# Kernel tuning notes

Hardware: AMD Instinct MI355X
Metric: run time of the kernel (lower is better)

The kernel has to match this reference:

```python
import jax, jax.numpy as jnp
import numpy as np
from jax import lax

B, T, D, R, V = 128, 8, 2048, 4, 512

def setup_inputs() -> dict:
    key = jax.random.key(0)
    k0, k1, k2, k3, k4 = jax.random.split(key, 5)
    # scales chosen so the TT products stay within fp32 range (see notes)
    input_embs = jax.random.normal(k0, (B, T, D), dtype=jnp.float32) * 0.1
    label_ids = jax.random.randint(k1, (B, T), 0, V)
    w_alpha = jax.random.normal(k2, (D, R), dtype=jnp.float32) * 0.04
    w_beta = jax.random.normal(k3, (D, R), dtype=jnp.float32) * 0.04
    w_vocab = jax.random.normal(k4, (D, V * R * R), dtype=jnp.float32) * 0.04
    return {"input_embs": input_embs, "label_ids": label_ids,
            "w_alpha": w_alpha, "w_beta": w_beta, "w_vocab": w_vocab}

def _tt_loss(input_embs, w_alpha, w_beta, w_vocab, label_ids):
    b, t, d = input_embs.shape
    flat = input_embs.reshape(-1, d)                    # [B*T, D]
    alpha = jnp.abs((flat @ w_alpha).reshape(b, t, R).mean(1))   # [B, R]
    beta = jnp.abs((flat @ w_beta).reshape(b, t, R).mean(1))     # [B, R]
    core = jnp.abs((flat @ w_vocab).reshape(b, t, R, V, R).mean(1))  # [B, R, V, R]

    # --- _select: gather per-position R x R cores and chain-multiply ---
    core_v = core.transpose(0, 2, 1, 3)                 # [B, V, R, R]
    sel = jnp.take_along_axis(core_v, label_ids[:, :, None, None], axis=1)  # [B, T, R, R]
    sel_t = jnp.swapaxes(sel, 0, 1)                     # [T, B, R, R]

    def chain(carry, m):
        return jnp.einsum('bik,bkj->bij', carry, m), None
    res, _ = lax.scan(chain, sel_t[0], sel_t[1:])       # [B, R, R]
    u = jnp.einsum('bi,bij,bj->b', alpha, res, beta)    # unnormalized probs [B]

    # --- normalization constant: marg^(T+1) contracted with alpha/beta ---
    marg = core.sum(2)                                  # [B, R, R]

    def pow_step(c, _):
        return jnp.einsum('bik,bkj->bij', c, marg), None
    zmat, _ = lax.scan(pow_step, marg, None, length=t)  # marg^(t+1)
    z = jnp.einsum('bi,bij,bj->b', alpha, zmat, beta)

    loss = -jnp.log(u / z)
    return loss.mean()

def reference(input_embs, label_ids, w_alpha, w_beta, w_vocab):
    return _tt_loss(input_embs, w_alpha, w_beta, w_vocab, label_ids)
```

## Files before the change

### kernel.cpp

```cpp
#include <hip/hip_runtime.h>
#include <math.h>

#define BB 128
#define TT 8
#define DD 2048
#define RR 4
#define VV 512

typedef __attribute__((ext_vector_type(8))) short short8;
typedef __attribute__((ext_vector_type(4))) float v4f;

#define BARSYNC() asm volatile("s_waitcnt lgkmcnt(0)\n\ts_barrier" ::: "memory")

__device__ __forceinline__ unsigned pack_bf16(float x, float y) {
    union { float f; unsigned u; } a, b;
    a.f = x; b.f = y;
    unsigned ua = a.u + 0x7fffu + ((a.u >> 16) & 1u);
    unsigned ub = b.u + 0x7fffu + ((b.u >> 16) & 1u);
    return (ua >> 16) | (ub & 0xffff0000u);
}

__global__ __launch_bounds__(256) void phaseA(const float* __restrict__ inp,
                                              const float* __restrict__ w_alpha,
                                              const float* __restrict__ w_beta,
                                              unsigned short* __restrict__ fmb,
                                              float* __restrict__ alphaP,
                                              float* __restrict__ betaP,
                                              float* __restrict__ marg) {
    int bid = blockIdx.x;
    int b = bid >> 1, half = bid & 1;
    int tid = threadIdx.x;

    if (bid < 8) marg[bid * 256 + tid] = 0.f;

    const float* base = inp + (size_t)b * TT * DD;
    float pa[4] = {0.f, 0.f, 0.f, 0.f};
    float pb[4] = {0.f, 0.f, 0.f, 0.f};
#pragma unroll
    for (int i = 0; i < 4; ++i) {
        int d = half * 1024 + i * 256 + tid;
        float s = 0.f;
#pragma unroll
        for (int t = 0; t < TT; ++t) s += base[t * DD + d];
        float v = s * (1.0f / TT);
        union { float f; unsigned u; } cv; cv.f = v;
        unsigned r = cv.u + 0x7fffu + ((cv.u >> 16) & 1u);
        fmb[b * DD + d] = (unsigned short)(r >> 16);
        float4 wa = *(const float4*)(w_alpha + d * 4);
        float4 wb = *(const float4*)(w_beta + d * 4);
        pa[0] += v * wa.x; pa[1] += v * wa.y; pa[2] += v * wa.z; pa[3] += v * wa.w;
        pb[0] += v * wb.x; pb[1] += v * wb.y; pb[2] += v * wb.z; pb[3] += v * wb.w;
    }
#pragma unroll
    for (int r = 0; r < 4; ++r) {
        for (int m = 1; m < 64; m <<= 1) {
            pa[r] += __shfl_xor(pa[r], m);
            pb[r] += __shfl_xor(pb[r], m);
        }
    }
    __shared__ float sA[4][4], sB[4][4];
    int wid = tid >> 6;
    if ((tid & 63) == 0) {
#pragma unroll
        for (int r = 0; r < 4; ++r) { sA[wid][r] = pa[r]; sB[wid][r] = pb[r]; }
    }
    __syncthreads();
    if (tid < 4) {
        alphaP[b * 8 + half * 4 + tid] = sA[0][tid] + sA[1][tid] + sA[2][tid] + sA[3][tid];
        betaP [b * 8 + half * 4 + tid] = sB[0][tid] + sB[1][tid] + sB[2][tid] + sB[3][tid];
    }
}

__global__ __launch_bounds__(512, 2) void phaseB(const unsigned short* __restrict__ fmb,
                                                 const float* __restrict__ wv,
                                                 const int* __restrict__ labels,
                                                 float* __restrict__ margA,
                                                 float* __restrict__ sel) {
    __shared__ unsigned short Ws[4][32][136];
    __shared__ int slab[BB * TT];

    const int tid = threadIdx.x;
    const int nb = blockIdx.x;
    const int col0 = nb * 32;

    slab[tid] = labels[tid];
    slab[tid + 512] = labels[tid + 512];

    const int nq = tid & 7;
    const int kp = tid >> 3;
    const int w = tid >> 6;
    const int lane = tid & 63;
    const int m15 = lane & 15;
    const int q = lane >> 4;

    const float* wbase = wv + (size_t)(2 * kp) * 8192 + col0 + nq * 4;
    const unsigned short* abase = fmb + (w * 16 + m15) * DD + q * 8;

    v4f acc0 = {0.f, 0.f, 0.f, 0.f};
    v4f acc1 = {0.f, 0.f, 0.f, 0.f};
    short8 afr[2][4];
    float4 sw[3][2];

#pragma unroll
    for (int c = 0; c < 3; ++c) {
        const float* p = wbase + (size_t)c * 128 * 8192;
        sw[c][0] = *(const float4*)(p);
        sw[c][1] = *(const float4*)(p + 8192);
    }
#pragma unroll
    for (int ks = 0; ks < 4; ++ks) afr[0][ks] = *(const short8*)(abase + ks * 32);
#pragma unroll
    for (int c = 0; c < 2; ++c) {
        const float* f0 = (const float*)&sw[c][0];
        const float* f1 = (const float*)&sw[c][1];
#pragma unroll
        for (int j = 0; j < 4; ++j)
            *(unsigned*)&Ws[c][nq * 4 + j][2 * kp] = pack_bf16(f0[j], f1[j]);
    }
    BARSYNC();

#pragma unroll
    for (int c = 0; c < 16; ++c) {
        if (c + 3 < 16) {
            const float* p = wbase + (size_t)(c + 3) * 128 * 8192;
            sw[c % 3][0] = *(const float4*)(p);
            sw[c % 3][1] = *(const float4*)(p + 8192);
        }
        if (c + 1 < 16) {
            const unsigned short* ap = abase + (c + 1) * 128;
#pragma unroll
            for (int ks = 0; ks < 4; ++ks) afr[(c + 1) & 1][ks] = *(const short8*)(ap + ks * 32);
        }
#pragma unroll
        for (int ks = 0; ks < 4; ++ks) {
            short8 b0 = *(const short8*)&Ws[c & 3][m15][ks * 32 + q * 8];
            short8 b1 = *(const short8*)&Ws[c & 3][16 + m15][ks * 32 + q * 8];
            acc0 = __builtin_amdgcn_mfma_f32_16x16x32_bf16(afr[c & 1][ks], b0, acc0, 0, 0, 0);
            acc1 = __builtin_amdgcn_mfma_f32_16x16x32_bf16(afr[c & 1][ks], b1, acc1, 0, 0, 0);
        }
        if (c + 2 < 16) {
            const float* f0 = (const float*)&sw[(c + 2) % 3][0];
            const float* f1 = (const float*)&sw[(c + 2) % 3][1];
#pragma unroll
            for (int j = 0; j < 4; ++j)
                *(unsigned*)&Ws[(c + 2) & 3][nq * 4 + j][2 * kp] = pack_bf16(f0[j], f1[j]);
        }
        if (c & 1) BARSYNC();
    }

    const int vbase = (nb & 63) * 8;
    const int iblk = nb >> 6;
    const int j = m15 & 3;
    const int v0 = vbase + (m15 >> 2);
    const float* a0p = (const float*)&acc0;
    const float* a1p = (const float*)&acc1;
#pragma unroll
    for (int r = 0; r < 4; ++r) {
        int m = w * 16 + q * 4 + r;
        float a0 = fabsf(a0p[r]);
        float a1 = fabsf(a1p[r]);
        float s = a0 + a1;
        s += __shfl_xor(s, 4);
        s += __shfl_xor(s, 8);
        if ((lane & 12) == 0) atomicAdd(&margA[m * 16 + iblk * 4 + j], s);
#pragma unroll
        for (int t = 0; t < TT; ++t) {
            int lv = slab[m * 8 + t];
            if (lv == v0)     sel[(m * 8 + t) * 16 + iblk * 4 + j] = a0;
            if (lv == v0 + 4) sel[(m * 8 + t) * 16 + iblk * 4 + j] = a1;
        }
    }
}

__global__ __launch_bounds__(128) void phaseD(const float* __restrict__ alphaP,
                                              const float* __restrict__ betaP,
                                              const float* __restrict__ marg,
                                              const float* __restrict__ sel,
                                              float* __restrict__ out) {
    int b = threadIdx.x;
    const float* sb = sel + b * TT * 16;
    float res[16], tmp[16], mm[16], zm[16];
#pragma unroll
    for (int e = 0; e < 16; ++e) res[e] = sb[e];
    for (int t = 1; t < TT; ++t) {
        const float* m = sb + t * 16;
#pragma unroll
        for (int i = 0; i < 4; ++i)
#pragma unroll
            for (int jj = 0; jj < 4; ++jj) {
                float s = 0.f;
#pragma unroll
                for (int k = 0; k < 4; ++k) s += res[i * 4 + k] * m[k * 4 + jj];
                tmp[i * 4 + jj] = s;
            }
#pragma unroll
        for (int e = 0; e < 16; ++e) res[e] = tmp[e];
    }
#pragma unroll
    for (int e = 0; e < 16; ++e) { mm[e] = marg[b * 16 + e]; zm[e] = mm[e]; }
    for (int st = 0; st < TT; ++st) {
#pragma unroll
        for (int i = 0; i < 4; ++i)
#pragma unroll
            for (int jj = 0; jj < 4; ++jj) {
                float s = 0.f;
#pragma unroll
                for (int k = 0; k < 4; ++k) s += zm[i * 4 + k] * mm[k * 4 + jj];
                tmp[i * 4 + jj] = s;
            }
#pragma unroll
        for (int e = 0; e < 16; ++e) zm[e] = tmp[e];
    }
    float u = 0.f, z = 0.f;
#pragma unroll
    for (int i = 0; i < 4; ++i) {
        float ai = fabsf(alphaP[b * 8 + i] + alphaP[b * 8 + 4 + i]);
#pragma unroll
        for (int jj = 0; jj < 4; ++jj) {
            float bj = fabsf(betaP[b * 8 + jj] + betaP[b * 8 + 4 + jj]);
            u += ai * res[i * 4 + jj] * bj;
            z += ai * zm[i * 4 + jj] * bj;
        }
    }
    float loss = logf(z) - logf(u);
    __shared__ float red[128];
    red[b] = loss;
    __syncthreads();
    for (int off = 64; off >= 1; off >>= 1) {
        if (b < off) red[b] += red[b + off];
        __syncthreads();
    }
    if (b == 0) out[0] = red[0] * (1.0f / BB);
}

extern "C" void kernel_launch(void* const* d_in, const int* in_sizes, int n_in,
                              void* d_out, int out_size, void* d_ws, size_t ws_size,
                              hipStream_t stream) {
    const float* inp     = (const float*)d_in[0];
    const int*   labels  = (const int*)d_in[1];
    const float* w_alpha = (const float*)d_in[2];
    const float* w_beta  = (const float*)d_in[3];
    const float* wv      = (const float*)d_in[4];
    float* out = (float*)d_out;

    float* ws     = (float*)d_ws;
    float* alphaP = ws;
    float* betaP  = ws + 1024;
    float* marg   = ws + 2048;
    float* sel    = ws + 4096;
    unsigned short* fmb = (unsigned short*)(ws + 20480);

    phaseA<<<256, 256, 0, stream>>>(inp, w_alpha, w_beta, fmb, alphaP, betaP, marg);
    phaseB<<<256, 512, 0, stream>>>(fmb, wv, labels, marg, sel);
    phaseD<<<1, 128, 0, stream>>>(alphaP, betaP, marg, sel, out);
}
```

Before: 124.4 us.

## Use inline-asm global loads with explicit vmcnt waits and double-buffered LDS

```diff
diff --git a/kernel.cpp b/kernel.cpp
--- a/kernel.cpp
+++ b/kernel.cpp
@@ -11,6 +11,13 @@
 typedef __attribute__((ext_vector_type(4))) float v4f;
 
 #define BARSYNC() asm volatile("s_waitcnt lgkmcnt(0)\n\ts_barrier" ::: "memory")
+
+__device__ __forceinline__ void gl4f(float4& d, const float* p) {
+    asm volatile("global_load_dwordx4 %0, %1, off" : "=v"(d) : "v"(p));
+}
+__device__ __forceinline__ void gl4s(short8& d, const unsigned short* p) {
+    asm volatile("global_load_dwordx4 %0, %1, off" : "=v"(d) : "v"(p));
+}
 
 __device__ __forceinline__ unsigned pack_bf16(float x, float y) {
     union { float f; unsigned u; } a, b;
@@ -76,7 +83,7 @@
                                                  const int* __restrict__ labels,
                                                  float* __restrict__ margA,
                                                  float* __restrict__ sel) {
-    __shared__ unsigned short Ws[4][32][136];
+    __shared__ unsigned short Ws[2][32][136];
     __shared__ int slab[BB * TT];
 
     const int tid = threadIdx.x;
@@ -99,53 +106,63 @@
     v4f acc0 = {0.f, 0.f, 0.f, 0.f};
     v4f acc1 = {0.f, 0.f, 0.f, 0.f};
     short8 afr[2][4];
-    float4 sw[3][2];
-
-#pragma unroll
-    for (int c = 0; c < 3; ++c) {
-        const float* p = wbase + (size_t)c * 128 * 8192;
-        sw[c][0] = *(const float4*)(p);
-        sw[c][1] = *(const float4*)(p + 8192);
-    }
-#pragma unroll
-    for (int ks = 0; ks < 4; ++ks) afr[0][ks] = *(const short8*)(abase + ks * 32);
-#pragma unroll
-    for (int c = 0; c < 2; ++c) {
-        const float* f0 = (const float*)&sw[c][0];
-        const float* f1 = (const float*)&sw[c][1];
+    float4 sw[2][2];
+
+    gl4f(sw[0][0], wbase);
+    gl4f(sw[0][1], wbase + 8192);
+    {
+        const float* p = wbase + (size_t)128 * 8192;
+        gl4f(sw[1][0], p);
+        gl4f(sw[1][1], p + 8192);
+    }
+#pragma unroll
+    for (int ks = 0; ks < 4; ++ks) gl4s(afr[0][ks], abase + ks * 32);
+
+    asm volatile("s_waitcnt vmcnt(6)" ::: "memory");
+    __builtin_amdgcn_sched_barrier(0);
+    {
+        const float* f0 = (const float*)&sw[0][0];
+        const float* f1 = (const float*)&sw[0][1];
 #pragma unroll
         for (int j = 0; j < 4; ++j)
-            *(unsigned*)&Ws[c][nq * 4 + j][2 * kp] = pack_bf16(f0[j], f1[j]);
+            *(unsigned*)&Ws[0][nq * 4 + j][2 * kp] = pack_bf16(f0[j], f1[j]);
     }
     BARSYNC();
 
 #pragma unroll
     for (int c = 0; c < 16; ++c) {
-        if (c + 3 < 16) {
-            const float* p = wbase + (size_t)(c + 3) * 128 * 8192;
-            sw[c % 3][0] = *(const float4*)(p);
-            sw[c % 3][1] = *(const float4*)(p + 8192);
+        const int P = c & 1, Q = 1 - P;
+        if (c + 2 < 16) {
+            const float* p = wbase + (size_t)(c + 2) * 128 * 8192;
+            gl4f(sw[P][0], p);
+            gl4f(sw[P][1], p + 8192);
         }
         if (c + 1 < 16) {
             const unsigned short* ap = abase + (c + 1) * 128;
-#pragma unroll
-            for (int ks = 0; ks < 4; ++ks) afr[(c + 1) & 1][ks] = *(const short8*)(ap + ks * 32);
-        }
+            gl4s(afr[Q][0], ap);
+            gl4s(afr[Q][1], ap + 32);
+            gl4s(afr[Q][2], ap + 64);
+            gl4s(afr[Q][3], ap + 96);
+        }
+        if (c <= 13)      asm volatile("s_waitcnt vmcnt(6)" ::: "memory");
+        else if (c == 14) asm volatile("s_waitcnt vmcnt(4)" ::: "memory");
+        else              asm volatile("s_waitcnt vmcnt(0)" ::: "memory");
+        __builtin_amdgcn_sched_barrier(0);
 #pragma unroll
         for (int ks = 0; ks < 4; ++ks) {
-            short8 b0 = *(const short8*)&Ws[c & 3][m15][ks * 32 + q * 8];
-            short8 b1 = *(const short8*)&Ws[c & 3][16 + m15][ks * 32 + q * 8];
-            acc0 = __builtin_amdgcn_mfma_f32_16x16x32_bf16(afr[c & 1][ks], b0, acc0, 0, 0, 0);
-            acc1 = __builtin_amdgcn_mfma_f32_16x16x32_bf16(afr[c & 1][ks], b1, acc1, 0, 0, 0);
-        }
-        if (c + 2 < 16) {
-            const float* f0 = (const float*)&sw[(c + 2) % 3][0];
-            const float* f1 = (const float*)&sw[(c + 2) % 3][1];
+            short8 b0 = *(const short8*)&Ws[P][m15][ks * 32 + q * 8];
+            short8 b1 = *(const short8*)&Ws[P][16 + m15][ks * 32 + q * 8];
+            acc0 = __builtin_amdgcn_mfma_f32_16x16x32_bf16(afr[P][ks], b0, acc0, 0, 0, 0);
+            acc1 = __builtin_amdgcn_mfma_f32_16x16x32_bf16(afr[P][ks], b1, acc1, 0, 0, 0);
+        }
+        if (c + 1 < 16) {
+            const float* f0 = (const float*)&sw[Q][0];
+            const float* f1 = (const float*)&sw[Q][1];
 #pragma unroll
             for (int j = 0; j < 4; ++j)
-                *(unsigned*)&Ws[(c + 2) & 3][nq * 4 + j][2 * kp] = pack_bf16(f0[j], f1[j]);
-        }
-        if (c & 1) BARSYNC();
+                *(unsigned*)&Ws[Q][nq * 4 + j][2 * kp] = pack_bf16(f0[j], f1[j]);
+        }
+        BARSYNC();
     }
 
     const int vbase = (nb & 63) * 8;
```

Result: no change. 122.4 us (-1.6%).
